# Kernel optimization log

Hardware: AMD Instinct MI355X
Metric: run time of the kernel (lower is better)

Reference implementation:

```python
import jax, jax.numpy as jnp
import numpy as np

K_TARGETS = 15  # hardcoded k in _select_targets
N_CLASSES = 8


def setup_inputs() -> dict:
    key = jax.random.key(0)
    k1, k2, k3 = jax.random.split(key, 3)
    n, p, d = 128, 512, 64
    return {
        "segment_center": jax.random.normal(k1, (n, d), dtype=jnp.float32),
        "outputs": jax.random.normal(k2, (n, p, d), dtype=jnp.float32),
        "label_inds": jax.random.randint(k3, (n, p), 0, N_CLASSES),
    }


def reference(segment_center, outputs, label_inds):
    # segment_center: [n, d]; outputs: [n, p, d]; label_inds: [n, p] int
    n, p, d = outputs.shape
    labels = label_inds.reshape(n, p)
    same = labels[:, :, None] == labels[:, None, :]          # [n, p, p] same-label mask

    # squared distance of each point to its segment center: cdist(...)^2
    dist_c = jnp.sum((outputs - segment_center[:, None, :]) ** 2, axis=-1)  # [n, p]

    # _select_targets: dd[n,i,j] = dist_c[n,i], masked to +inf where labels differ,
    # topk smallest over j -> k same-label target-neighbor indices per point.
    dd = jnp.where(same, dist_c[:, :, None], jnp.inf)        # [n, p, p]
    _, target_neighbors = jax.lax.top_k(-dd, K_TARGETS)      # [n, p, K] smallest

    # squared center-distance of each target neighbor (intended gather in forward)
    gathered = dist_c[jnp.arange(n)[:, None, None], target_neighbors]  # [n, p, K]

    furthest = gathered.max(axis=2)                          # [n, p]
    margin_radii = 1.0 + furthest                            # per-point margin
    pull_loss = gathered.sum()

    # _find_impostors: per-segment margin = 1 + max center-dist over all gathered
    # target neighbors; impostor (n,i,j) iff label_i != label_j and
    # dist_c[n,i] < margin_seg[n]. Hinge term depends only on (n,i), so sum the
    # hinge weighted by the count of different-label j (avoids nonzero/gather).
    margin_seg = 1.0 + gathered.max(axis=(1, 2))             # [n]
    diff_count = (p - same.sum(axis=2)).astype(outputs.dtype)  # [n, p] #{j: label_j != label_i}
    is_impostor = (dist_c < margin_seg[:, None]).astype(outputs.dtype)  # [n, p]
    hinge = jnp.maximum(margin_radii - dist_c, 0.0)          # [n, p]
    push_loss = jnp.sum(diff_count * is_impostor * hinge)

    return (pull_loss + push_loss) / (n * p)
```

## Files before the change

### kernel.cpp

```cpp
#include <hip/hip_runtime.h>
#include <math.h>

constexpr int NSEG = 128;
constexpr int P    = 512;
constexpr int D    = 64;
constexpr int KT   = 15;
constexpr int NCLS = 8;

__global__ __launch_bounds__(256) void dist_kernel(
    const float* __restrict__ center,
    const float* __restrict__ outputs,
    float* __restrict__ dist,
    float* __restrict__ out)
{
    if (blockIdx.x == 0 && threadIdx.x == 0) out[0] = 0.0f;

    const int seg     = blockIdx.x >> 2;
    const int quarter = blockIdx.x & 3;
    const int t   = threadIdx.x;
    const int sub = t & 15;
    const int pg  = t >> 4;

    const float4* c4 = reinterpret_cast<const float4*>(center);
    const float4  cf = c4[seg * 16 + sub];

    const float4* o4 = reinterpret_cast<const float4*>(outputs);
    const int pt_base = quarter * 128;

    #pragma unroll
    for (int it = 0; it < 8; ++it) {
        const int pt = pt_base + it * 16 + pg;
        float4 v = o4[((size_t)seg * P + pt) * 16 + sub];
        float dx = v.x - cf.x;
        float dy = v.y - cf.y;
        float dz = v.z - cf.z;
        float dw = v.w - cf.w;
        float acc = dx * dx + dy * dy + dz * dz + dw * dw;
        acc += __shfl_xor(acc, 1);
        acc += __shfl_xor(acc, 2);
        acc += __shfl_xor(acc, 4);
        acc += __shfl_xor(acc, 8);
        if (sub == 0) dist[seg * P + pt] = acc;
    }
}

__global__ __launch_bounds__(512, 1) void combine_kernel(
    const float* __restrict__ dist,
    const int*   __restrict__ labels,
    float* __restrict__ out)
{
    __shared__ float s_dist[P];
    __shared__ int   s_lab[P];
    __shared__ float s_S[NCLS];
    __shared__ float s_M[NCLS];
    __shared__ int   s_cnt[NCLS];
    __shared__ float s_hb[NCLS];
    __shared__ float s_dc[NCLS];
    __shared__ float s_margin;
    __shared__ float s_pull;
    __shared__ float s_wsum[8];

    const int seg  = blockIdx.x;
    const int tid  = threadIdx.x;
    const int lane = tid & 63;
    const int wave = tid >> 6;

    s_lab[tid]  = labels[seg * P + tid];
    s_dist[tid] = dist[seg * P + tid];
    __syncthreads();

    {
        const int c = wave;
        float S = 0.0f;
        float M = -INFINITY;
        int taken = 0;
        int total = 0;
        for (int j = 0; j < 8; ++j) {
            const int pos = j * 64 + lane;
            const bool pred = (s_lab[pos] == c);
            const unsigned long long mask = __ballot(pred);
            const int cnt  = __popcll(mask);
            const int rank = __popcll(mask & ((1ull << lane) - 1ull));
            const bool sel = pred && (taken + rank < KT);
            float vs = sel ? s_dist[pos] : 0.0f;
            float vm = sel ? s_dist[pos] : -INFINITY;
            #pragma unroll
            for (int m = 1; m < 64; m <<= 1) {
                vs += __shfl_xor(vs, m);
                vm = fmaxf(vm, __shfl_xor(vm, m));
            }
            S += vs;
            M = fmaxf(M, vm);
            total += cnt;
            taken += cnt;
            if (taken > KT) taken = KT;
        }
        if (total < KT) {
            const int need = KT - total;
            int t2 = 0;
            for (int j = 0; j < 8 && t2 < need; ++j) {
                const int pos = j * 64 + lane;
                const bool pred = (s_lab[pos] != c);
                const unsigned long long mask = __ballot(pred);
                const int cnt  = __popcll(mask);
                const int rank = __popcll(mask & ((1ull << lane) - 1ull));
                const bool sel = pred && (t2 + rank < need);
                float vs = sel ? s_dist[pos] : 0.0f;
                float vm = sel ? s_dist[pos] : -INFINITY;
                #pragma unroll
                for (int m = 1; m < 64; m <<= 1) {
                    vs += __shfl_xor(vs, m);
                    vm = fmaxf(vm, __shfl_xor(vm, m));
                }
                S += vs;
                M = fmaxf(M, vm);
                t2 += cnt;
                if (t2 > need) t2 = need;
            }
        }
        if (lane == 0) {
            s_S[c]   = S;
            s_M[c]   = M;
            s_cnt[c] = total;
        }
    }
    __syncthreads();

    if (tid == 0) {
        float margin = -INFINITY;
        float pull = 0.0f;
        for (int c = 0; c < NCLS; ++c) {
            if (s_cnt[c] > 0) margin = fmaxf(margin, s_M[c]);
            pull += (float)s_cnt[c] * s_S[c];
            s_hb[c] = 1.0f + s_M[c];
            s_dc[c] = (float)(P - s_cnt[c]);
        }
        s_margin = 1.0f + margin;
        s_pull = pull;
    }
    __syncthreads();

    {
        const float dv = s_dist[tid];
        const int   c  = s_lab[tid];
        const float h  = fmaxf(s_hb[c] - dv, 0.0f);
        float v = (dv < s_margin) ? s_dc[c] * h : 0.0f;
        #pragma unroll
        for (int m = 1; m < 64; m <<= 1) v += __shfl_xor(v, m);
        if (lane == 0) s_wsum[wave] = v;
    }
    __syncthreads();

    if (tid == 0) {
        float t = s_pull;
        #pragma unroll
        for (int w = 0; w < 8; ++w) t += s_wsum[w];
        atomicAdd(out, t * (1.0f / ((float)NSEG * (float)P)));
    }
}

extern "C" void kernel_launch(void* const* d_in, const int* in_sizes, int n_in,
                              void* d_out, int out_size, void* d_ws, size_t ws_size,
                              hipStream_t stream) {
    const float* center  = (const float*)d_in[0];
    const float* outputs = (const float*)d_in[1];
    const int*   labels  = (const int*)d_in[2];
    float* out  = (float*)d_out;
    float* dist = (float*)d_ws;

    dist_kernel<<<dim3(NSEG * 4), dim3(256), 0, stream>>>(center, outputs, dist, out);
    combine_kernel<<<dim3(NSEG), dim3(512), 0, stream>>>(dist, labels, out);
}
```

Baseline: 74.76 us.

## Fuse distance and combine kernels with last-block-done atomic counters

```diff
diff --git a/kernel.cpp b/kernel.cpp
--- a/kernel.cpp
+++ b/kernel.cpp
@@ -1,5 +1,6 @@
 #include <hip/hip_runtime.h>
 #include <math.h>
+#include <stdint.h>
 
 constexpr int NSEG = 128;
 constexpr int P    = 512;
@@ -7,46 +8,14 @@
 constexpr int KT   = 15;
 constexpr int NCLS = 8;
 
-__global__ __launch_bounds__(256) void dist_kernel(
+constexpr size_t CTRL_OFF = (size_t)1 << 20;
+constexpr size_t CTRL_ZERO_BYTES = (NSEG * 16 + 16) * sizeof(uint32_t);
+
+__global__ __launch_bounds__(512, 1) void lmnn_fused(
     const float* __restrict__ center,
     const float* __restrict__ outputs,
-    float* __restrict__ dist,
-    float* __restrict__ out)
-{
-    if (blockIdx.x == 0 && threadIdx.x == 0) out[0] = 0.0f;
-
-    const int seg     = blockIdx.x >> 2;
-    const int quarter = blockIdx.x & 3;
-    const int t   = threadIdx.x;
-    const int sub = t & 15;
-    const int pg  = t >> 4;
-
-    const float4* c4 = reinterpret_cast<const float4*>(center);
-    const float4  cf = c4[seg * 16 + sub];
-
-    const float4* o4 = reinterpret_cast<const float4*>(outputs);
-    const int pt_base = quarter * 128;
-
-    #pragma unroll
-    for (int it = 0; it < 8; ++it) {
-        const int pt = pt_base + it * 16 + pg;
-        float4 v = o4[((size_t)seg * P + pt) * 16 + sub];
-        float dx = v.x - cf.x;
-        float dy = v.y - cf.y;
-        float dz = v.z - cf.z;
-        float dw = v.w - cf.w;
-        float acc = dx * dx + dy * dy + dz * dz + dw * dw;
-        acc += __shfl_xor(acc, 1);
-        acc += __shfl_xor(acc, 2);
-        acc += __shfl_xor(acc, 4);
-        acc += __shfl_xor(acc, 8);
-        if (sub == 0) dist[seg * P + pt] = acc;
-    }
-}
-
-__global__ __launch_bounds__(512, 1) void combine_kernel(
-    const float* __restrict__ dist,
     const int*   __restrict__ labels,
+    float* __restrict__ ws,
     float* __restrict__ out)
 {
     __shared__ float s_dist[P];
@@ -59,11 +28,53 @@
     __shared__ float s_margin;
     __shared__ float s_pull;
     __shared__ float s_wsum[8];
-
-    const int seg  = blockIdx.x;
+    __shared__ int   s_flag;
+
+    const int bid  = blockIdx.x;
+    const int seg  = bid >> 1;
+    const int half = bid & 1;
     const int tid  = threadIdx.x;
     const int lane = tid & 63;
     const int wave = tid >> 6;
+
+    float*    dist    = ws;
+    uint32_t* ctrl    = reinterpret_cast<uint32_t*>(reinterpret_cast<char*>(ws) + CTRL_OFF);
+    uint32_t* qcnt    = ctrl;
+    uint32_t* ccnt    = ctrl + NSEG * 16;
+    float*    partial = reinterpret_cast<float*>(ctrl + (NSEG + 2) * 16);
+
+    {
+        const int sub = tid & 15;
+        const int pg  = tid >> 4;
+        const float4 cf = reinterpret_cast<const float4*>(center)[seg * 16 + sub];
+        const float4* o4 = reinterpret_cast<const float4*>(outputs);
+        const int pt_base = half * 256;
+        #pragma unroll
+        for (int it = 0; it < 8; ++it) {
+            const int pt = pt_base + it * 32 + pg;
+            float4 v = o4[((size_t)seg * P + pt) * 16 + sub];
+            float dx = v.x - cf.x;
+            float dy = v.y - cf.y;
+            float dz = v.z - cf.z;
+            float dw = v.w - cf.w;
+            float acc = dx * dx + dy * dy + dz * dz + dw * dw;
+            acc += __shfl_xor(acc, 1);
+            acc += __shfl_xor(acc, 2);
+            acc += __shfl_xor(acc, 4);
+            acc += __shfl_xor(acc, 8);
+            if (sub == 0) dist[seg * P + pt] = acc;
+        }
+    }
+
+    __syncthreads();
+    if (tid == 0) {
+        __threadfence();
+        uint32_t old = __hip_atomic_fetch_add(&qcnt[seg * 16], 1u,
+                           __ATOMIC_ACQ_REL, __HIP_MEMORY_SCOPE_AGENT);
+        s_flag = (old == 1u);
+    }
+    __syncthreads();
+    if (!s_flag) return;
 
     s_lab[tid]  = labels[seg * P + tid];
     s_dist[tid] = dist[seg * P + tid];
@@ -155,7 +166,24 @@
         float t = s_pull;
         #pragma unroll
         for (int w = 0; w < 8; ++w) t += s_wsum[w];
-        atomicAdd(out, t * (1.0f / ((float)NSEG * (float)P)));
+        partial[seg] = t * (1.0f / ((float)NSEG * (float)P));
+        __threadfence();
+        uint32_t old = __hip_atomic_fetch_add(ccnt, 1u,
+                           __ATOMIC_ACQ_REL, __HIP_MEMORY_SCOPE_AGENT);
+        s_flag = (old == (uint32_t)(NSEG - 1));
+    }
+    __syncthreads();
+    if (!s_flag) return;
+
+    if (tid < 64) {
+        float v = partial[tid] + partial[tid + 64];
+        v += __shfl_xor(v, 1);
+        v += __shfl_xor(v, 2);
+        v += __shfl_xor(v, 4);
+        v += __shfl_xor(v, 8);
+        v += __shfl_xor(v, 16);
+        v += __shfl_xor(v, 32);
+        if (tid == 0) out[0] = v;
     }
 }
 
@@ -165,9 +193,9 @@
     const float* center  = (const float*)d_in[0];
     const float* outputs = (const float*)d_in[1];
     const int*   labels  = (const int*)d_in[2];
-    float* out  = (float*)d_out;
-    float* dist = (float*)d_ws;
-
-    dist_kernel<<<dim3(NSEG * 4), dim3(256), 0, stream>>>(center, outputs, dist, out);
-    combine_kernel<<<dim3(NSEG), dim3(512), 0, stream>>>(dist, labels, out);
+    float* out = (float*)d_out;
+    float* ws  = (float*)d_ws;
+
+    hipMemsetAsync((char*)d_ws + CTRL_OFF, 0, CTRL_ZERO_BYTES, stream);
+    lmnn_fused<<<dim3(NSEG * 2), dim3(512), 0, stream>>>(center, outputs, labels, ws, out);
 }
```

Result: slower. 88.34 us (+18.2%).

## Fuse distance computation into per-segment kernel and replace atomics with final reduce

Applied to the files above, without the earlier changes.

```diff
diff --git a/kernel.cpp b/kernel.cpp
--- a/kernel.cpp
+++ b/kernel.cpp
@@ -1,5 +1,6 @@
 #include <hip/hip_runtime.h>
 #include <math.h>
+#include <stdint.h>
 
 constexpr int NSEG = 128;
 constexpr int P    = 512;
@@ -7,47 +8,11 @@
 constexpr int KT   = 15;
 constexpr int NCLS = 8;
 
-__global__ __launch_bounds__(256) void dist_kernel(
+__global__ __launch_bounds__(1024, 1) void lmnn_seg_kernel(
     const float* __restrict__ center,
     const float* __restrict__ outputs,
-    float* __restrict__ dist,
-    float* __restrict__ out)
-{
-    if (blockIdx.x == 0 && threadIdx.x == 0) out[0] = 0.0f;
-
-    const int seg     = blockIdx.x >> 2;
-    const int quarter = blockIdx.x & 3;
-    const int t   = threadIdx.x;
-    const int sub = t & 15;
-    const int pg  = t >> 4;
-
-    const float4* c4 = reinterpret_cast<const float4*>(center);
-    const float4  cf = c4[seg * 16 + sub];
-
-    const float4* o4 = reinterpret_cast<const float4*>(outputs);
-    const int pt_base = quarter * 128;
-
-    #pragma unroll
-    for (int it = 0; it < 8; ++it) {
-        const int pt = pt_base + it * 16 + pg;
-        float4 v = o4[((size_t)seg * P + pt) * 16 + sub];
-        float dx = v.x - cf.x;
-        float dy = v.y - cf.y;
-        float dz = v.z - cf.z;
-        float dw = v.w - cf.w;
-        float acc = dx * dx + dy * dy + dz * dz + dw * dw;
-        acc += __shfl_xor(acc, 1);
-        acc += __shfl_xor(acc, 2);
-        acc += __shfl_xor(acc, 4);
-        acc += __shfl_xor(acc, 8);
-        if (sub == 0) dist[seg * P + pt] = acc;
-    }
-}
-
-__global__ __launch_bounds__(512, 1) void combine_kernel(
-    const float* __restrict__ dist,
     const int*   __restrict__ labels,
-    float* __restrict__ out)
+    float* __restrict__ partial)
 {
     __shared__ float s_dist[P];
     __shared__ int   s_lab[P];
@@ -65,14 +30,35 @@
     const int lane = tid & 63;
     const int wave = tid >> 6;
 
-    s_lab[tid]  = labels[seg * P + tid];
-    s_dist[tid] = dist[seg * P + tid];
+    if (tid < P) s_lab[tid] = labels[seg * P + tid];
+
+    {
+        const int sub = tid & 15;
+        const int pg  = tid >> 4;
+        const float4 cf = reinterpret_cast<const float4*>(center)[seg * 16 + sub];
+        const float4* o4 = reinterpret_cast<const float4*>(outputs);
+        #pragma unroll
+        for (int it = 0; it < 8; ++it) {
+            const int pt = it * 64 + pg;
+            float4 v = o4[((size_t)seg * P + pt) * 16 + sub];
+            float dx = v.x - cf.x;
+            float dy = v.y - cf.y;
+            float dz = v.z - cf.z;
+            float dw = v.w - cf.w;
+            float acc = dx * dx + dy * dy + dz * dz + dw * dw;
+            acc += __shfl_xor(acc, 1);
+            acc += __shfl_xor(acc, 2);
+            acc += __shfl_xor(acc, 4);
+            acc += __shfl_xor(acc, 8);
+            if (sub == 0) s_dist[pt] = acc;
+        }
+    }
     __syncthreads();
 
-    {
+    if (wave < NCLS) {
         const int c = wave;
         float S = 0.0f;
-        float M = -INFINITY;
+        float vmLane = -INFINITY;
         int taken = 0;
         int total = 0;
         for (int j = 0; j < 8; ++j) {
@@ -83,14 +69,10 @@
             const int rank = __popcll(mask & ((1ull << lane) - 1ull));
             const bool sel = pred && (taken + rank < KT);
             float vs = sel ? s_dist[pos] : 0.0f;
-            float vm = sel ? s_dist[pos] : -INFINITY;
+            if (sel) vmLane = fmaxf(vmLane, s_dist[pos]);
             #pragma unroll
-            for (int m = 1; m < 64; m <<= 1) {
-                vs += __shfl_xor(vs, m);
-                vm = fmaxf(vm, __shfl_xor(vm, m));
-            }
+            for (int m = 1; m < 64; m <<= 1) vs += __shfl_xor(vs, m);
             S += vs;
-            M = fmaxf(M, vm);
             total += cnt;
             taken += cnt;
             if (taken > KT) taken = KT;
@@ -106,18 +88,17 @@
                 const int rank = __popcll(mask & ((1ull << lane) - 1ull));
                 const bool sel = pred && (t2 + rank < need);
                 float vs = sel ? s_dist[pos] : 0.0f;
-                float vm = sel ? s_dist[pos] : -INFINITY;
+                if (sel) vmLane = fmaxf(vmLane, s_dist[pos]);
                 #pragma unroll
-                for (int m = 1; m < 64; m <<= 1) {
-                    vs += __shfl_xor(vs, m);
-                    vm = fmaxf(vm, __shfl_xor(vm, m));
-                }
+                for (int m = 1; m < 64; m <<= 1) vs += __shfl_xor(vs, m);
                 S += vs;
-                M = fmaxf(M, vm);
                 t2 += cnt;
                 if (t2 > need) t2 = need;
             }
         }
+        float M = vmLane;
+        #pragma unroll
+        for (int m = 1; m < 64; m <<= 1) M = fmaxf(M, __shfl_xor(M, m));
         if (lane == 0) {
             s_S[c]   = S;
             s_M[c]   = M;
@@ -140,7 +121,7 @@
     }
     __syncthreads();
 
-    {
+    if (tid < P) {
         const float dv = s_dist[tid];
         const int   c  = s_lab[tid];
         const float h  = fmaxf(s_hb[c] - dv, 0.0f);
@@ -155,8 +136,23 @@
         float t = s_pull;
         #pragma unroll
         for (int w = 0; w < 8; ++w) t += s_wsum[w];
-        atomicAdd(out, t * (1.0f / ((float)NSEG * (float)P)));
+        partial[seg] = t * (1.0f / ((float)NSEG * (float)P));
     }
+}
+
+__global__ __launch_bounds__(64) void final_reduce_kernel(
+    const float* __restrict__ partial,
+    float* __restrict__ out)
+{
+    const int tid = threadIdx.x;
+    float v = partial[tid] + partial[tid + 64];
+    v += __shfl_xor(v, 1);
+    v += __shfl_xor(v, 2);
+    v += __shfl_xor(v, 4);
+    v += __shfl_xor(v, 8);
+    v += __shfl_xor(v, 16);
+    v += __shfl_xor(v, 32);
+    if (tid == 0) out[0] = v;
 }
 
 extern "C" void kernel_launch(void* const* d_in, const int* in_sizes, int n_in,
@@ -165,9 +161,9 @@
     const float* center  = (const float*)d_in[0];
     const float* outputs = (const float*)d_in[1];
     const int*   labels  = (const int*)d_in[2];
-    float* out  = (float*)d_out;
-    float* dist = (float*)d_ws;
+    float* out     = (float*)d_out;
+    float* partial = (float*)d_ws;
 
-    dist_kernel<<<dim3(NSEG * 4), dim3(256), 0, stream>>>(center, outputs, dist, out);
-    combine_kernel<<<dim3(NSEG), dim3(512), 0, stream>>>(dist, labels, out);
+    lmnn_seg_kernel<<<dim3(NSEG), dim3(1024), 0, stream>>>(center, outputs, labels, partial);
+    final_reduce_kernel<<<dim3(1), dim3(64), 0, stream>>>(partial, out);
 }
```

Result: faster. 73.17 us (-2.1%).
